# Kernel optimization log

Measured on AMD Instinct MI355X. Metric: run time of the kernel, lower is better.

The kernel has to match this reference:

```python
import jax, jax.numpy as jnp
import numpy as np

EPS = 1e-6

# SIM(3) layout per lietorch: [tx,ty,tz, qx,qy,qz,qw, s]

def quat_mul(q1, q2):
    x1, y1, z1, w1 = jnp.moveaxis(q1, -1, 0)
    x2, y2, z2, w2 = jnp.moveaxis(q2, -1, 0)
    return jnp.stack([
        w1 * x2 + x1 * w2 + y1 * z2 - z1 * y2,
        w1 * y2 - x1 * z2 + y1 * w2 + z1 * x2,
        w1 * z2 + x1 * y2 - y1 * x2 + z1 * w2,
        w1 * w2 - x1 * x2 - y1 * y2 - z1 * z2,
    ], axis=-1)


def quat_rotate(q, v):
    qv, qw = q[..., :3], q[..., 3:4]
    uv = jnp.cross(qv, v)
    return v + 2.0 * (qw * uv + jnp.cross(qv, uv))


def sim3_inv(T):
    t, q, s = T[..., :3], T[..., 3:7], T[..., 7:8]
    q_inv = q * jnp.array([-1.0, -1.0, -1.0, 1.0], dtype=T.dtype)
    s_inv = 1.0 / s
    t_inv = -s_inv * quat_rotate(q_inv, t)
    return jnp.concatenate([t_inv, q_inv, s_inv], axis=-1)


def sim3_mul(T1, T2):
    t1, q1, s1 = T1[..., :3], T1[..., 3:7], T1[..., 7:8]
    t2, q2, s2 = T2[..., :3], T2[..., 3:7], T2[..., 7:8]
    t = t1 + s1 * quat_rotate(q1, t2)
    return jnp.concatenate([t, quat_mul(q1, q2), s1 * s2], axis=-1)


def skew(v):
    x, y, z = v[..., 0], v[..., 1], v[..., 2]
    O = jnp.zeros_like(x)
    return jnp.stack([
        jnp.stack([O, -z, y], -1),
        jnp.stack([z, O, -x], -1),
        jnp.stack([-y, x, O], -1),
    ], -2)


def sim3_log(T):
    t, q, s = T[..., :3], T[..., 3:7], T[..., 7:8]
    qv, qw = q[..., :3], q[..., 3:4]
    nv = jnp.linalg.norm(qv, axis=-1, keepdims=True)
    theta_r = 2.0 * jnp.arctan2(nv, qw)  # rotation angle
    small_r = nv < EPS
    fac = jnp.where(small_r, 2.0, theta_r / jnp.where(small_r, 1.0, nv))
    phi = fac * qv  # so(3) log
    sigma = jnp.log(s)

    # W = C*I + A*Phi + B*Phi^2 (Sophus/lietorch Sim3 calcW), tau = W^{-1} t
    theta = jnp.linalg.norm(phi, axis=-1, keepdims=True)
    sig_small = jnp.abs(sigma) < EPS
    th_small = theta < EPS
    sg = jnp.where(sig_small, 1.0, sigma)
    th = jnp.where(th_small, 1.0, theta)
    scale = jnp.exp(sigma)
    th2, sg2 = th * th, sg * sg
    C = jnp.where(sig_small, 1.0, (scale - 1.0) / sg)
    # sigma ~ 0 branch
    A_ss = jnp.where(th_small, 0.5, (1.0 - jnp.cos(th)) / th2)
    B_ss = jnp.where(th_small, 1.0 / 6.0, (th - jnp.sin(th)) / (th2 * th))
    # generic branch
    a = scale * jnp.sin(th)
    b = scale * jnp.cos(th)
    c = th2 + sg2
    A_g = (a * sg + (1.0 - b) * th) / (th * c)
    B_g = (C - ((b - 1.0) * sg + a * th) / c) / th2
    # theta ~ 0, sigma not small branch
    A_ts = ((sg - 1.0) * scale + 1.0) / sg2
    B_ts = (scale * (sg2 - 2.0 * sg + 2.0) - 2.0) / (2.0 * sg2 * sg)
    A = jnp.where(sig_small, A_ss, jnp.where(th_small, A_ts, A_g))
    B = jnp.where(sig_small, B_ss, jnp.where(th_small, B_ts, B_g))

    Phi = skew(phi)
    I3 = jnp.eye(3, dtype=T.dtype)
    W = C[..., None] * I3 + A[..., None] * Phi + B[..., None] * (Phi @ Phi)
    tau = jnp.linalg.solve(W, t[..., None])[..., 0]
    return jnp.concatenate([tau, phi, sigma], axis=-1)


def _rand_sim3(key, n):
    k1, k2, k3 = jax.random.split(key, 3)
    t = jax.random.normal(k1, (n, 3), dtype=jnp.float32)
    q = jax.random.normal(k2, (n, 4), dtype=jnp.float32)
    q = q / jnp.linalg.norm(q, axis=-1, keepdims=True)
    q = jnp.where(q[:, 3:4] < 0, -q, q)  # w >= 0
    s = jnp.exp(0.1 * jax.random.normal(k3, (n, 1), dtype=jnp.float32))
    return jnp.concatenate([t, q, s], axis=-1)


N_FRAME = 1_000_000
N_LC = N_FRAME - 1


def setup_inputs() -> dict:
    key = jax.random.key(0)
    ks = jax.random.split(key, 7)
    return {
        "Twc": _rand_sim3(ks[0], N_FRAME),
        "Twc_prior_inv": _rand_sim3(ks[1], N_FRAME - 1),
        "Todom_inv": _rand_sim3(ks[2], N_FRAME - 1),
        "prior_weight": jax.random.uniform(ks[3], (N_FRAME - 1, 7), dtype=jnp.float32),
        "odom_weight": jax.random.uniform(ks[4], (N_FRAME - 1, 7), dtype=jnp.float32),
        "edges": jax.random.randint(ks[5], (N_LC, 2), 0, N_FRAME),
        "T_lc": _rand_sim3(ks[6], N_LC),
    }


def reference(Twc, Twc_prior_inv, Todom_inv, prior_weight, odom_weight, edges, T_lc):
    Ti_inv = sim3_inv(Twc[:-1])
    delta = sim3_mul(Ti_inv, Twc[1:])  # Twc[:-1].Inv() * Twc[1:]
    r_prior = sim3_log(sim3_mul(delta, Twc_prior_inv)) * prior_weight
    # NOTE: source uses self.odom_Twc[1:]; in this module only self.Twc exists,
    # so odom delta uses the same pose chain.
    r_odom = sim3_log(sim3_mul(delta, Todom_inv)) * odom_weight
    residual = r_prior + r_odom
    # loop closures: gather poses by edge indices
    delta_lc = sim3_mul(sim3_inv(Twc[edges[:, 0]]), Twc[edges[:, 1]])
    r_lc = sim3_log(sim3_mul(delta_lc, T_lc))
    return residual + r_lc
```

## Files before the change

### kernel.cpp

```cpp
#include <hip/hip_runtime.h>
#include <math.h>

#define EPSF 1e-6f

struct F3   { float x, y, z; };
struct Quat { float x, y, z, w; };
struct Sim3 { F3 t; Quat q; float s; };

__device__ __forceinline__ F3 cross3(F3 a, F3 b) {
    return { a.y*b.z - a.z*b.y, a.z*b.x - a.x*b.z, a.x*b.y - a.y*b.x };
}

__device__ __forceinline__ F3 quat_rotate(Quat q, F3 v) {
    F3 qv { q.x, q.y, q.z };
    F3 uv  = cross3(qv, v);
    F3 cuv = cross3(qv, uv);
    return { v.x + 2.0f*(q.w*uv.x + cuv.x),
             v.y + 2.0f*(q.w*uv.y + cuv.y),
             v.z + 2.0f*(q.w*uv.z + cuv.z) };
}

__device__ __forceinline__ Quat quat_mul(Quat a, Quat b) {
    return {
        a.w*b.x + a.x*b.w + a.y*b.z - a.z*b.y,
        a.w*b.y - a.x*b.z + a.y*b.w + a.z*b.x,
        a.w*b.z + a.x*b.y - a.y*b.x + a.z*b.w,
        a.w*b.w - a.x*b.x - a.y*b.y - a.z*b.z
    };
}

__device__ __forceinline__ Sim3 sim3_inv(Sim3 T) {
    Quat qi { -T.q.x, -T.q.y, -T.q.z, T.q.w };
    float si = 1.0f / T.s;
    F3 r = quat_rotate(qi, T.t);
    return { { -si*r.x, -si*r.y, -si*r.z }, qi, si };
}

__device__ __forceinline__ Sim3 sim3_mul(Sim3 A, Sim3 B) {
    F3 r = quat_rotate(A.q, B.t);
    return { { A.t.x + A.s*r.x, A.t.y + A.s*r.y, A.t.z + A.s*r.z },
             quat_mul(A.q, B.q), A.s * B.s };
}

__device__ __forceinline__ Sim3 load_sim3(const float* __restrict__ p) {
    float4 a = *reinterpret_cast<const float4*>(p);
    float4 b = *reinterpret_cast<const float4*>(p + 4);
    return { {a.x, a.y, a.z}, {a.w, b.x, b.y, b.z}, b.w };
}

__device__ __forceinline__ void sim3_log(Sim3 T, float out[7]) {
    float qx = T.q.x, qy = T.q.y, qz = T.q.z, qw = T.q.w;
    float nv = sqrtf(qx*qx + qy*qy + qz*qz);
    float theta_r = 2.0f * atan2f(nv, qw);
    float fac = (nv < EPSF) ? 2.0f : (theta_r / nv);
    float px = fac*qx, py = fac*qy, pz = fac*qz;
    float sigma = logf(T.s);
    float theta = sqrtf(px*px + py*py + pz*pz);

    bool sig_small = fabsf(sigma) < EPSF;
    bool th_small  = theta < EPSF;
    float sg = sig_small ? 1.0f : sigma;
    float th = th_small  ? 1.0f : theta;
    float scale = expf(sigma);
    float th2 = th*th, sg2 = sg*sg;
    float C = sig_small ? 1.0f : (scale - 1.0f) / sg;
    float sth = sinf(th), cth = cosf(th);
    float A_ss = th_small ? 0.5f : (1.0f - cth) / th2;
    float B_ss = th_small ? (1.0f/6.0f) : (th - sth) / (th2 * th);
    float a = scale * sth;
    float b = scale * cth;
    float c = th2 + sg2;
    float A_g = (a*sg + (1.0f - b)*th) / (th * c);
    float B_g = (C - ((b - 1.0f)*sg + a*th) / c) / th2;
    float A_ts = ((sg - 1.0f)*scale + 1.0f) / sg2;
    float B_ts = (scale*(sg2 - 2.0f*sg + 2.0f) - 2.0f) / (2.0f*sg2*sg);
    float A = sig_small ? A_ss : (th_small ? A_ts : A_g);
    float B = sig_small ? B_ss : (th_small ? B_ts : B_g);

    float P01 = -pz, P02 =  py;
    float P10 =  pz, P12 = -px;
    float P20 = -py, P21 =  px;
    float Q00 = P01*P10 + P02*P20;
    float Q01 = P02*P21;
    float Q02 = P01*P12;
    float Q10 = P12*P20;
    float Q11 = P10*P01 + P12*P21;
    float Q12 = P10*P02;
    float Q20 = P21*P10;
    float Q21 = P20*P01;
    float Q22 = P20*P02 + P21*P12;

    float W00 = C + B*Q00,          W01 = A*P01 + B*Q01, W02 = A*P02 + B*Q02;
    float W10 = A*P10 + B*Q10,      W11 = C + B*Q11,     W12 = A*P12 + B*Q12;
    float W20 = A*P20 + B*Q20,      W21 = A*P21 + B*Q21, W22 = C + B*Q22;

    double d00=W00, d01=W01, d02=W02, d10=W10, d11=W11, d12=W12, d20=W20, d21=W21, d22=W22;
    double c00 = d11*d22 - d12*d21;
    double c01 = d12*d20 - d10*d22;
    double c02 = d10*d21 - d11*d20;
    double det = d00*c00 + d01*c01 + d02*c02;
    double idet = 1.0 / det;
    double tx = T.t.x, ty = T.t.y, tz = T.t.z;
    out[0] = (float)((c00*tx + (d02*d21 - d01*d22)*ty + (d01*d12 - d02*d11)*tz) * idet);
    out[1] = (float)((c01*tx + (d00*d22 - d02*d20)*ty + (d02*d10 - d00*d12)*tz) * idet);
    out[2] = (float)((c02*tx + (d01*d20 - d00*d21)*ty + (d00*d11 - d01*d10)*tz) * idet);
    out[3] = px; out[4] = py; out[5] = pz; out[6] = sigma;
}

__global__ void __launch_bounds__(256) pgo_kernel(
        const float* __restrict__ Twc,
        const float* __restrict__ Tp_inv,
        const float* __restrict__ To_inv,
        const float* __restrict__ pw,
        const float* __restrict__ ow,
        const int*   __restrict__ edges,
        const float* __restrict__ T_lc,
        float*       __restrict__ out,
        int n) {
    int i = blockIdx.x * blockDim.x + threadIdx.x;
    if (i >= n) return;
    size_t i8 = (size_t)i * 8;
    size_t i7 = (size_t)i * 7;

    Sim3 Ti = load_sim3(Twc + i8);
    Sim3 Tj = load_sim3(Twc + i8 + 8);
    Sim3 delta = sim3_mul(sim3_inv(Ti), Tj);

    float rp[7], ro[7], rl[7];
    sim3_log(sim3_mul(delta, load_sim3(Tp_inv + i8)), rp);
    sim3_log(sim3_mul(delta, load_sim3(To_inv + i8)), ro);

    int e0 = edges[2*(size_t)i];
    int e1 = edges[2*(size_t)i + 1];
    Sim3 dlc = sim3_mul(sim3_inv(load_sim3(Twc + (size_t)e0 * 8)),
                        load_sim3(Twc + (size_t)e1 * 8));
    sim3_log(sim3_mul(dlc, load_sim3(T_lc + i8)), rl);

    #pragma unroll
    for (int k = 0; k < 7; ++k) {
        out[i7 + k] = rp[k]*pw[i7 + k] + ro[k]*ow[i7 + k] + rl[k];
    }
}

extern "C" void kernel_launch(void* const* d_in, const int* in_sizes, int n_in,
                              void* d_out, int out_size, void* d_ws, size_t ws_size,
                              hipStream_t stream) {
    const float* Twc   = (const float*)d_in[0];
    const float* Tp    = (const float*)d_in[1];
    const float* To    = (const float*)d_in[2];
    const float* pw    = (const float*)d_in[3];
    const float* ow    = (const float*)d_in[4];
    const int*   edges = (const int*)d_in[5];
    const float* Tlc   = (const float*)d_in[6];
    float* out = (float*)d_out;

    int n = in_sizes[1] / 8;
    const int block = 256;
    int grid = (n + block - 1) / block;
    pgo_kernel<<<grid, block, 0, stream>>>(Twc, Tp, To, pw, ow, edges, Tlc, out, n);
}
```

Baseline: 215.5 us.

## Replace libm transcendentals and double inverse with fast float math, hoist loads

```diff
diff --git a/kernel.cpp b/kernel.cpp
--- a/kernel.cpp
+++ b/kernel.cpp
@@ -6,6 +6,8 @@
 struct F3   { float x, y, z; };
 struct Quat { float x, y, z, w; };
 struct Sim3 { F3 t; Quat q; float s; };
+
+__device__ __forceinline__ float frcp(float x) { return __builtin_amdgcn_rcpf(x); }
 
 __device__ __forceinline__ F3 cross3(F3 a, F3 b) {
     return { a.y*b.z - a.z*b.y, a.z*b.x - a.x*b.z, a.x*b.y - a.y*b.x };
@@ -31,7 +33,7 @@
 
 __device__ __forceinline__ Sim3 sim3_inv(Sim3 T) {
     Quat qi { -T.q.x, -T.q.y, -T.q.z, T.q.w };
-    float si = 1.0f / T.s;
+    float si = frcp(T.s);
     F3 r = quat_rotate(qi, T.t);
     return { { -si*r.x, -si*r.y, -si*r.z }, qi, si };
 }
@@ -48,32 +50,57 @@
     return { {a.x, a.y, a.z}, {a.w, b.x, b.y, b.z}, b.w };
 }
 
+__device__ __forceinline__ float fast_atan2_pos(float y, float x) {
+    float ax = fabsf(x);
+    float mn = fminf(ax, y), mx = fmaxf(ax, y);
+    float t  = mn * frcp(mx);
+    float t2 = t * t;
+    float p = fmaf(t2, -0.0117212f,  0.05265332f);
+    p = fmaf(t2, p, -0.11643287f);
+    p = fmaf(t2, p,  0.19354346f);
+    p = fmaf(t2, p, -0.33262347f);
+    p = fmaf(t2, p,  0.99997726f);
+    float r = t * p;
+    r = (y > ax)   ? 1.57079632679f - r : r;
+    r = (x < 0.0f) ? 3.14159265359f - r : r;
+    return r;
+}
+
 __device__ __forceinline__ void sim3_log(Sim3 T, float out[7]) {
     float qx = T.q.x, qy = T.q.y, qz = T.q.z, qw = T.q.w;
-    float nv = sqrtf(qx*qx + qy*qy + qz*qz);
-    float theta_r = 2.0f * atan2f(nv, qw);
-    float fac = (nv < EPSF) ? 2.0f : (theta_r / nv);
+    float nv2 = fmaf(qx, qx, fmaf(qy, qy, qz*qz));
+    float nv  = sqrtf(nv2);
+    float theta_r = 2.0f * fast_atan2_pos(nv, qw);
+    float fac = (nv < EPSF) ? 2.0f : theta_r * frcp(nv);
     float px = fac*qx, py = fac*qy, pz = fac*qz;
-    float sigma = logf(T.s);
-    float theta = sqrtf(px*px + py*py + pz*pz);
+    float sigma = __logf(T.s);
+    float theta = sqrtf(fmaf(px, px, fmaf(py, py, pz*pz)));
 
     bool sig_small = fabsf(sigma) < EPSF;
     bool th_small  = theta < EPSF;
     float sg = sig_small ? 1.0f : sigma;
     float th = th_small  ? 1.0f : theta;
-    float scale = expf(sigma);
+    float scale = __expf(sigma);
     float th2 = th*th, sg2 = sg*sg;
-    float C = sig_small ? 1.0f : (scale - 1.0f) / sg;
-    float sth = sinf(th), cth = cosf(th);
-    float A_ss = th_small ? 0.5f : (1.0f - cth) / th2;
-    float B_ss = th_small ? (1.0f/6.0f) : (th - sth) / (th2 * th);
+    float rsg  = frcp(sg);
+    float rth2 = frcp(th2);
+    float C = sig_small ? 1.0f : (scale - 1.0f) * rsg;
+
+    float inv_q = frcp(nv2 + qw*qw);
+    float sth = 2.0f * qw * nv * inv_q;
+    float cth = (qw*qw - nv2) * inv_q;
+
+    float A_ss = th_small ? 0.5f        : (1.0f - cth) * rth2;
+    float B_ss = th_small ? (1.0f/6.0f) : (th - sth) * frcp(th2 * th);
     float a = scale * sth;
     float b = scale * cth;
     float c = th2 + sg2;
-    float A_g = (a*sg + (1.0f - b)*th) / (th * c);
-    float B_g = (C - ((b - 1.0f)*sg + a*th) / c) / th2;
-    float A_ts = ((sg - 1.0f)*scale + 1.0f) / sg2;
-    float B_ts = (scale*(sg2 - 2.0f*sg + 2.0f) - 2.0f) / (2.0f*sg2*sg);
+    float rc = frcp(c);
+    float A_g = fmaf(a, sg, (1.0f - b)*th) * frcp(th * c);
+    float B_g = (C - fmaf(b - 1.0f, sg, a*th) * rc) * rth2;
+    float rsg2 = rsg * rsg;
+    float A_ts = fmaf(sg - 1.0f, scale, 1.0f) * rsg2;
+    float B_ts = fmaf(scale, fmaf(sg, sg - 2.0f, 2.0f), -2.0f) * (0.5f * rsg2 * rsg);
     float A = sig_small ? A_ss : (th_small ? A_ts : A_g);
     float B = sig_small ? B_ss : (th_small ? B_ts : B_g);
 
@@ -90,20 +117,31 @@
     float Q21 = P20*P01;
     float Q22 = P20*P02 + P21*P12;
 
-    float W00 = C + B*Q00,          W01 = A*P01 + B*Q01, W02 = A*P02 + B*Q02;
-    float W10 = A*P10 + B*Q10,      W11 = C + B*Q11,     W12 = A*P12 + B*Q12;
-    float W20 = A*P20 + B*Q20,      W21 = A*P21 + B*Q21, W22 = C + B*Q22;
-
-    double d00=W00, d01=W01, d02=W02, d10=W10, d11=W11, d12=W12, d20=W20, d21=W21, d22=W22;
-    double c00 = d11*d22 - d12*d21;
-    double c01 = d12*d20 - d10*d22;
-    double c02 = d10*d21 - d11*d20;
-    double det = d00*c00 + d01*c01 + d02*c02;
-    double idet = 1.0 / det;
-    double tx = T.t.x, ty = T.t.y, tz = T.t.z;
-    out[0] = (float)((c00*tx + (d02*d21 - d01*d22)*ty + (d01*d12 - d02*d11)*tz) * idet);
-    out[1] = (float)((c01*tx + (d00*d22 - d02*d20)*ty + (d02*d10 - d00*d12)*tz) * idet);
-    out[2] = (float)((c02*tx + (d01*d20 - d00*d21)*ty + (d00*d11 - d01*d10)*tz) * idet);
+    float W00 = fmaf(B, Q00, C);
+    float W01 = fmaf(A, P01, B*Q01);
+    float W02 = fmaf(A, P02, B*Q02);
+    float W10 = fmaf(A, P10, B*Q10);
+    float W11 = fmaf(B, Q11, C);
+    float W12 = fmaf(A, P12, B*Q12);
+    float W20 = fmaf(A, P20, B*Q20);
+    float W21 = fmaf(A, P21, B*Q21);
+    float W22 = fmaf(B, Q22, C);
+
+    float c00 = fmaf(W11, W22, -W12*W21);
+    float c01 = fmaf(W12, W20, -W10*W22);
+    float c02 = fmaf(W10, W21, -W11*W20);
+    float det = fmaf(W00, c00, fmaf(W01, c01, W02*c02));
+    float idet = frcp(det);
+    float m01 = fmaf(W02, W21, -W01*W22);
+    float m02 = fmaf(W01, W12, -W02*W11);
+    float m11 = fmaf(W00, W22, -W02*W20);
+    float m12 = fmaf(W02, W10, -W00*W12);
+    float m21 = fmaf(W01, W20, -W00*W21);
+    float m22 = fmaf(W00, W11, -W01*W10);
+    float tx = T.t.x, ty = T.t.y, tz = T.t.z;
+    out[0] = fmaf(c00, tx, fmaf(m01, ty, m02*tz)) * idet;
+    out[1] = fmaf(c01, tx, fmaf(m11, ty, m12*tz)) * idet;
+    out[2] = fmaf(c02, tx, fmaf(m21, ty, m22*tz)) * idet;
     out[3] = px; out[4] = py; out[5] = pz; out[6] = sigma;
 }
 
@@ -122,23 +160,25 @@
     size_t i8 = (size_t)i * 8;
     size_t i7 = (size_t)i * 7;
 
+    int2 e = *reinterpret_cast<const int2*>(edges + 2*(size_t)i);
+    Sim3 Ta = load_sim3(Twc + (size_t)e.x * 8);
+    Sim3 Tb = load_sim3(Twc + (size_t)e.y * 8);
     Sim3 Ti = load_sim3(Twc + i8);
     Sim3 Tj = load_sim3(Twc + i8 + 8);
+    Sim3 Tp = load_sim3(Tp_inv + i8);
+    Sim3 To = load_sim3(To_inv + i8);
+    Sim3 Tl = load_sim3(T_lc + i8);
+
     Sim3 delta = sim3_mul(sim3_inv(Ti), Tj);
 
     float rp[7], ro[7], rl[7];
-    sim3_log(sim3_mul(delta, load_sim3(Tp_inv + i8)), rp);
-    sim3_log(sim3_mul(delta, load_sim3(To_inv + i8)), ro);
-
-    int e0 = edges[2*(size_t)i];
-    int e1 = edges[2*(size_t)i + 1];
-    Sim3 dlc = sim3_mul(sim3_inv(load_sim3(Twc + (size_t)e0 * 8)),
-                        load_sim3(Twc + (size_t)e1 * 8));
-    sim3_log(sim3_mul(dlc, load_sim3(T_lc + i8)), rl);
+    sim3_log(sim3_mul(delta, Tp), rp);
+    sim3_log(sim3_mul(delta, To), ro);
+    sim3_log(sim3_mul(sim3_mul(sim3_inv(Ta), Tb), Tl), rl);
 
     #pragma unroll
     for (int k = 0; k < 7; ++k) {
-        out[i7 + k] = rp[k]*pw[i7 + k] + ro[k]*ow[i7 + k] + rl[k];
+        out[i7 + k] = fmaf(rp[k], pw[i7 + k], fmaf(ro[k], ow[i7 + k], rl[k]));
     }
 }
 
```

Result: no change. 217.9 us (+1.1%).
